# Optimization experiments

Measured on AMD Instinct MI355X. Metric: run time of the kernel, lower is better.

Reference implementation:

```python
import jax, jax.numpy as jnp
import numpy as np

EMBED = 3072
HEADS = 24
HEAD_DIM = EMBED // HEADS
FFN = 4 * EMBED
SEGS = (1024, 2048, 4096)
DILS = (1, 2, 4)
SEQ = 8192
BATCH = 1


def setup_inputs() -> dict:
    key = jax.random.key(0)
    ks = jax.random.split(key, 8)
    E, F = EMBED, FFN
    s = lambda k, shape, sc: (jax.random.normal(k, shape, jnp.float32) * sc)
    return {
        "x": s(ks[0], (BATCH, SEQ, E), 1.0),
        "expert_embed": s(ks[1], (1, 1, E), 0.02),
        "w_qkv": s(ks[2], (3 * E, E), E ** -0.5),
        "b_qkv": jnp.zeros((3 * E,), jnp.float32),
        "w_out": s(ks[3], (E, E), E ** -0.5),
        "b_out": jnp.zeros((E,), jnp.float32),
        "ln1_g": jnp.ones((E,), jnp.float32),
        "ln1_b": jnp.zeros((E,), jnp.float32),
        "w1": s(ks[4], (F, E), E ** -0.5),
        "b1": jnp.zeros((F,), jnp.float32),
        "w2": s(ks[5], (E, F), F ** -0.5),
        "b2": jnp.zeros((E,), jnp.float32),
        "ln2_g": jnp.ones((E,), jnp.float32),
        "ln2_b": jnp.zeros((E,), jnp.float32),
    }


def _layernorm(x, g, b):
    m = jnp.mean(x, axis=-1, keepdims=True)
    v = jnp.mean(jnp.square(x - m), axis=-1, keepdims=True)
    return (x - m) * jax.lax.rsqrt(v + 1e-5) * g + b


def _dilated_attn(q, k, v):
    # q,k,v: [b, n, h, d]; heads are partitioned across dilation groups
    b, n, h, d = q.shape
    G = len(SEGS)
    hg = h // G
    scale = 1.0 / np.sqrt(d)
    outs = []
    for i, (g, r) in enumerate(zip(SEGS, DILS)):
        off = i % r
        hs = slice(i * hg, (i + 1) * hg)

        def sel(t):
            # [b, n, h, d] -> [b, n//g, g//r, hg, d] (dilated segment view)
            return t.reshape(b, n // g, g, h, d)[:, :, off::r, hs, :]

        qi, ki, vi = sel(q), sel(k), sel(v)
        att = jnp.einsum("bsqhd,bskhd->bshqk", qi, ki) * scale
        att = jax.nn.softmax(att, axis=-1)
        oi = jnp.einsum("bshqk,bskhd->bsqhd", att, vi)
        # scatter dilated positions back; unselected positions stay zero
        buf = jnp.zeros((b, n // g, g, hg, d), q.dtype).at[:, :, off::r].set(oi)
        outs.append(buf.reshape(b, n, hg, d))
    return jnp.concatenate(outs, axis=2)  # head groups are contiguous slices


def reference(x, expert_embed, w_qkv, b_qkv, w_out, b_out,
              ln1_g, ln1_b, w1, b1, w2, b2, ln2_g, ln2_b):
    b, n, E = x.shape
    x = x + expert_embed
    qkv = x @ w_qkv.T + b_qkv
    q, k, v = [t.reshape(b, n, HEADS, HEAD_DIM) for t in jnp.split(qkv, 3, axis=-1)]
    a = _dilated_attn(q, k, v).reshape(b, n, E) @ w_out.T + b_out
    x = _layernorm(x + a, ln1_g, ln1_b)
    f = jax.nn.gelu(x @ w1.T + b1, approximate=False) @ w2.T + b2
    return _layernorm(x + f, ln2_g, ln2_b)
```

## Files before the change

kernel.cpp:

```cpp
#include <hip/hip_runtime.h>

typedef unsigned short u16;
typedef __bf16 bf16x8 __attribute__((ext_vector_type(8)));
typedef float f32x4 __attribute__((ext_vector_type(4)));
typedef u16 u16x4 __attribute__((ext_vector_type(4)));
typedef u16 u16x8 __attribute__((ext_vector_type(8)));

__device__ __forceinline__ u16 f2bf(float f) {
  union { float f; unsigned u; } v; v.f = f;
  return (u16)((v.u + 0x7fffu + ((v.u >> 16) & 1u)) >> 16);
}
__device__ __forceinline__ float b2f(u16 h) {
  union { unsigned u; float f; } v; v.u = ((unsigned)h) << 16; return v.f;
}

__device__ __forceinline__ void gld16(const void* g, void* l) {
  __builtin_amdgcn_global_load_lds(
      (const __attribute__((address_space(1))) unsigned int*)g,
      (__attribute__((address_space(3))) unsigned int*)l, 16, 0, 0);
}

#define BAR() asm volatile("s_barrier" ::: "memory")
#define VMC6() asm volatile("s_waitcnt vmcnt(6)" ::: "memory")
#define VMC0() asm volatile("s_waitcnt vmcnt(0)" ::: "memory")

__global__ __launch_bounds__(256) void prep_kernel(const float* __restrict__ x,
                                                   const float* __restrict__ ee,
                                                   u16* __restrict__ xb) {
  size_t i = ((size_t)blockIdx.x * 256 + threadIdx.x) * 4;
  int col = (int)(i % 3072);
  f32x4 v = *(const f32x4*)&x[i];
  f32x4 e = *(const f32x4*)&ee[col];
  v += e;
  u16x4 b = { f2bf(v[0]), f2bf(v[1]), f2bf(v[2]), f2bf(v[3]) };
  *(u16x4*)&xb[i] = b;
}

__global__ __launch_bounds__(256) void cvt_kernel(const float* __restrict__ in,
                                                  u16* __restrict__ out, size_t n) {
  size_t i = ((size_t)blockIdx.x * 256 + threadIdx.x) * 4;
  if (i >= n) return;
  f32x4 v = *(const f32x4*)&in[i];
  u16x4 b = { f2bf(v[0]), f2bf(v[1]), f2bf(v[2]), f2bf(v[3]) };
  *(u16x4*)&out[i] = b;
}

__global__ __launch_bounds__(256) void cvt_strided_kernel(const float* __restrict__ in,
                                                          u16* __restrict__ out, int k0) {
  size_t i = ((size_t)blockIdx.x * 256 + threadIdx.x) * 4;
  int n = (int)(i / 6144), k = (int)(i % 6144);
  f32x4 v = *(const f32x4*)&in[(size_t)n * 12288 + k0 + k];
  u16x4 b = { f2bf(v[0]), f2bf(v[1]), f2bf(v[2]), f2bf(v[3]) };
  *(u16x4*)&out[i] = b;
}

template<int EPI>
__global__ __launch_bounds__(512, 2) void gemmu_kernel(const u16* __restrict__ A,
                                                       const u16* __restrict__ B,
                                                       const float* __restrict__ bias,
                                                       const float* __restrict__ residf,
                                                       const u16* __restrict__ residb,
                                                       const float* __restrict__ ee,
                                                       void* __restrict__ C0,
                                                       void* __restrict__ C1,
                                                       int N, int K) {
  __shared__ __align__(16) u16 lds[73728];
  const int tid = threadIdx.x;
  const int lane = tid & 63;
  const int w = tid >> 6;
  const int lr = lane & 15, lc8 = (lane >> 4) * 8;
  const int wm64 = (w >> 1) * 64;
  const int wn64 = (w & 1) * 64;
  const int rsw = (lr & 7) << 3;

  const int ntile = N >> 7;
  int bid = blockIdx.x;
  int wg = (bid & 7) * (gridDim.x >> 3) + (bid >> 3);
  const int bm = wg / ntile, bn = wg % ntile;
  const size_t m0 = (size_t)bm << 8, n0 = (size_t)bn << 7;

  const int jsw = (tid & 7) ^ ((tid >> 3) & 7);
  const u16* gA = A + (m0 + (tid >> 3)) * (size_t)K + jsw * 8;
  const u16* gB = B + (n0 + (tid >> 3)) * (size_t)K + jsw * 8;
  u16* lA = &lds[tid * 8];
  u16* lB = &lds[16384 + tid * 8];

  f32x4 acc[4][4] = {};
  bf16x8 af[2][4], bfr[2][4];

  const int NT = K >> 6;

  auto stageA2 = [&](int buf, int kk) {
    gld16(gA + kk, lA + buf * 24576);
    gld16(gA + (size_t)64 * K + kk, lA + buf * 24576 + 64 * 64);
    gld16(gA + (size_t)128 * K + kk, lA + buf * 24576 + 128 * 64);
    gld16(gA + (size_t)192 * K + kk, lA + buf * 24576 + 192 * 64);
  };
  auto stageB2 = [&](int buf, int kk) {
    gld16(gB + kk, lB + buf * 24576);
    gld16(gB + (size_t)64 * K + kk, lB + buf * 24576 + 64 * 64);
  };
  auto LA = [&](int buf) {
#pragma unroll
    for (int ks = 0; ks < 2; ++ks)
#pragma unroll
      for (int f = 0; f < 4; ++f) {
        int r = wm64 + f * 16 + lr;
        af[ks][f] = *(const bf16x8*)&lds[buf * 24576 + r * 64 + ((ks * 32 + lc8) ^ rsw)];
      }
  };
  auto LBall = [&](int buf) {
#pragma unroll
    for (int ks = 0; ks < 2; ++ks)
#pragma unroll
      for (int f = 0; f < 4; ++f) {
        int r = wn64 + f * 16 + lr;
        bfr[ks][f] = *(const bf16x8*)&lds[buf * 24576 + 16384 + r * 64 + ((ks * 32 + lc8) ^ rsw)];
      }
  };
  auto MMA = [&]() {
    __builtin_amdgcn_s_setprio(1);
#pragma unroll
    for (int ks = 0; ks < 2; ++ks)
#pragma unroll
      for (int f = 0; f < 4; ++f)
#pragma unroll
        for (int f2 = 0; f2 < 4; ++f2)
          acc[f][f2] = __builtin_amdgcn_mfma_f32_16x16x32_bf16(
              af[ks][f], bfr[ks][f2], acc[f][f2], 0, 0, 0);
    __builtin_amdgcn_s_setprio(0);
  };
  auto TILE = [&](int bc, int bs, int tt) {
    const int kk2 = (tt + 2) << 6;
    const bool p = (tt + 2) < NT;
    LA(bc); LBall(bc);
    if (p) { stageA2(bs, kk2); stageB2(bs, kk2); }
    MMA();
    if (p) { VMC6(); } else { VMC0(); }
    BAR();
  };

  stageA2(0, 0); stageB2(0, 0);
  stageA2(1, 64); stageB2(1, 64);
  VMC6();
  BAR();

  for (int t = 0; t < NT; t += 3) {
    TILE(0, 2, t);
    TILE(1, 0, t + 1);
    TILE(2, 1, t + 2);
  }

  const int ldc = (EPI == 7) ? 3072 : N;
#pragma unroll
  for (int nf = 0; nf < 4; ++nf) {
    const int colL = wn64 + nf * 16 + lr;
    const size_t col = n0 + colL;
    float bv = 0.f;
    if constexpr (EPI != 9) bv = bias[col];
    const int ci = colL >> 3;
#pragma unroll
    for (int f = 0; f < 4; ++f) {
#pragma unroll
      for (int rg = 0; rg < 4; ++rg) {
        const int rowL = wm64 + f * 16 + (lc8 >> 1) + rg;
        const size_t idx = (m0 + rowL) * (size_t)N + col;
        float v = acc[f][nf][rg] + bv;
        if constexpr (EPI == 2)
          v = 0.5f * v * (1.0f + erff(v * 0.7071067811865476f));
        if constexpr (EPI == 3) v += residf[idx] + ee[col];
        if constexpr (EPI == 8) v += b2f(residb[idx]);
        if constexpr (EPI == 9) v += b2f(((const u16*)C0)[idx]);
        const int fz = (rowL >> 2) & 7;
        lds[rowL * 128 + (((ci ^ fz) << 3) | (colL & 7))] = f2bf(v);
      }
    }
  }
  __syncthreads();
  const int row = tid >> 1, half = tid & 1;
  const int fro = (row >> 2) & 7;
  u16* dst;
  size_t cb;
  if constexpr (EPI == 7) {
    const int sec = (n0 >= 3072);
    dst = sec ? (u16*)C1 : (u16*)C0;
    cb = n0 - (sec ? 3072 : 0);
  } else {
    dst = (u16*)C0; cb = n0;
  }
  u16* gout = dst + (m0 + row) * (size_t)ldc + cb + half * 64;
#pragma unroll
  for (int i = 0; i < 8; ++i) {
    const int ci = half * 8 + i;
    *(uint4*)&gout[i * 8] = *(const uint4*)&lds[row * 128 + ((ci ^ fro) << 3)];
  }
}

__device__ __forceinline__ void decode_blk(int bid, int& grp, int& g, int& r, int& off,
                                           int& q16, int& hl, int& s) {
  if (bid < 1024)      { grp = 0; g = 1024; r = 1; off = 0; }
  else if (bid < 1536) { grp = 1; g = 2048; r = 2; off = 1; bid -= 1024; }
  else                 { grp = 2; g = 4096; r = 4; off = 2; bid -= 1536; }
  q16 = bid & 15; hl = (bid >> 4) & 7; s = bid >> 7;
}

__global__ __launch_bounds__(256) void vtrans_kernel(const u16* __restrict__ Vb,
                                                     u16* __restrict__ vtd) {
  int grp, g, r, off, jb, hl, s;
  decode_blk(blockIdx.x, grp, g, r, off, jb, hl, s);
  const int h = grp * 8 + hl;
  const size_t vbase = (size_t)((grp == 0) ? 0u : (grp == 1) ? 8388608u : 12582912u)
                       + (size_t)(s * 8 + hl) * 131072;
  __shared__ u16 t[64 * 128];
  const int tid = threadIdx.x;
#pragma unroll
  for (int i = 0; i < 4; ++i) {
    int c = tid + i * 256;
    int jj = c >> 4, c16 = c & 15;
    size_t pos = (size_t)s * g + off + (size_t)(jb * 64 + jj) * r;
    uint4 d = *(const uint4*)&Vb[pos * 3072 + h * 128 + c16 * 8];
    *(uint4*)((char*)t + jj * 256 + ((c16 * 16) ^ ((jj >> 3) << 4))) = d;
  }
  __syncthreads();
#pragma unroll
  for (int i = 0; i < 4; ++i) {
    int c = tid + i * 256;
    int dd = c >> 3, jc = c & 7;
    u16x8 vals;
#pragma unroll
    for (int q = 0; q < 8; ++q) {
      int row = jc * 8 + q;
      vals[q] = *(const u16*)((const char*)t + row * 256 + ((dd * 2) ^ (jc << 4)));
    }
    *(u16x8*)&vtd[vbase + (size_t)dd * 1024 + jb * 64 + jc * 8] = vals;
  }
}

__global__ __launch_bounds__(256) void attn_kernel(const u16* __restrict__ Qb,
                                                   const u16* __restrict__ Kb,
                                                   const u16* __restrict__ vtd,
                                                   u16* __restrict__ abuf) {
  int grp, g, r, off, qt, hl, s;
  decode_blk(blockIdx.x, grp, g, r, off, qt, hl, s);
  const int h = grp * 8 + hl;
  const size_t vbase = (size_t)((grp == 0) ? 0u : (grp == 1) ? 8388608u : 12582912u)
                       + (size_t)(s * 8 + hl) * 131072;
  const size_t segoff = (size_t)s * g + off;

  const int tid = threadIdx.x;
  const int lane = tid & 63, w = tid >> 6;
  const int lr = lane & 15, lc = lane >> 4;

  __shared__ u16 Kl[64 * 128];
  __shared__ u16 Vl[128 * 64];
  __shared__ u16 Pl[4][1024];

  const size_t qpos = segoff + (size_t)(qt * 64 + w * 16 + lr) * r;
  const u16* qrow = &Qb[qpos * 3072 + h * 128];
  bf16x8 qf[4];
#pragma unroll
  for (int kc = 0; kc < 4; ++kc) qf[kc] = *(const bf16x8*)&qrow[kc * 32 + lc * 8];

  float m_run[4], l_run[4];
  f32x4 ao[8] = {};
#pragma unroll
  for (int i = 0; i < 4; ++i) { m_run[i] = -1e30f; l_run[i] = 0.f; }

  const float scale = 0.08838834764831845f;

  for (int kt = 0; kt < 16; ++kt) {
    __syncthreads();
#pragma unroll
    for (int i = 0; i < 4; ++i) {
      int c = tid + i * 256;
      int jj = c >> 4, c16 = c & 15;
      size_t kpos = segoff + (size_t)(kt * 64 + jj) * r;
      uint4 kd = *(const uint4*)&Kb[kpos * 3072 + h * 128 + c16 * 8];
      *(uint4*)((char*)Kl + jj * 256 + ((c16 * 16) ^ ((jj & 7) << 4))) = kd;
      int dd = c >> 3, jc = c & 7;
      uint4 vd = *(const uint4*)&vtd[vbase + (size_t)dd * 1024 + kt * 64 + jc * 8];
      *(uint4*)((char*)Vl + dd * 128 + ((jc * 16) ^ ((dd & 7) << 4))) = vd;
    }
    __syncthreads();

    f32x4 sc4[4] = {};
#pragma unroll
    for (int kb = 0; kb < 4; ++kb) {
      const int key = kb * 16 + lr;
      const int swz = (key & 7) << 4;
#pragma unroll
      for (int kc = 0; kc < 4; ++kc) {
        bf16x8 kf = *(const bf16x8*)((const char*)Kl + key * 256 + ((kc * 64 + lc * 16) ^ swz));
        sc4[kb] = __builtin_amdgcn_mfma_f32_16x16x32_bf16(qf[kc], kf, sc4[kb], 0, 0, 0);
      }
    }

    float pv[4][4];
#pragma unroll
    for (int rg = 0; rg < 4; ++rg) {
      float t = fmaxf(fmaxf(sc4[0][rg], sc4[1][rg]), fmaxf(sc4[2][rg], sc4[3][rg]));
#pragma unroll
      for (int sh = 1; sh < 16; sh <<= 1) t = fmaxf(t, __shfl_xor(t, sh, 64));
      t *= scale;
      const float mn = fmaxf(m_run[rg], t);
      const float corr = __expf(m_run[rg] - mn);
      m_run[rg] = mn;
      float sum = 0.f;
#pragma unroll
      for (int kb = 0; kb < 4; ++kb) {
        float p = __expf(sc4[kb][rg] * scale - mn);
        pv[kb][rg] = p; sum += p;
      }
#pragma unroll
      for (int sh = 1; sh < 16; sh <<= 1) sum += __shfl_xor(sum, sh, 64);
      l_run[rg] = l_run[rg] * corr + sum;
#pragma unroll
      for (int nb = 0; nb < 8; ++nb) ao[nb][rg] *= corr;
    }

#pragma unroll
    for (int rg = 0; rg < 4; ++rg) {
      const int q = lc * 4 + rg;
      const int swq = (q & 7) << 4;
#pragma unroll
      for (int kb = 0; kb < 4; ++kb) {
        const int key = kb * 16 + lr;
        *(u16*)((char*)&Pl[w][0] + q * 128 + ((key * 2) ^ swq)) = f2bf(pv[kb][rg]);
      }
    }
    __syncthreads();

#pragma unroll
    for (int kc2 = 0; kc2 < 2; ++kc2) {
      bf16x8 pf = *(const bf16x8*)((const char*)&Pl[w][0] + lr * 128 + ((kc2 * 64 + lc * 16) ^ ((lr & 7) << 4)));
#pragma unroll
      for (int nb = 0; nb < 8; ++nb) {
        const int dd = nb * 16 + lr;
        bf16x8 vf = *(const bf16x8*)((const char*)Vl + dd * 128 + ((kc2 * 64 + lc * 16) ^ ((dd & 7) << 4)));
        ao[nb] = __builtin_amdgcn_mfma_f32_16x16x32_bf16(pf, vf, ao[nb], 0, 0, 0);
      }
    }
  }

#pragma unroll
  for (int rg = 0; rg < 4; ++rg) {
    const float inv = 1.f / l_run[rg];
    const size_t opos = segoff + (size_t)(qt * 64 + w * 16 + lc * 4 + rg) * r;
    u16* orow = &abuf[opos * 3072 + h * 128];
#pragma unroll
    for (int nb = 0; nb < 8; ++nb) orow[nb * 16 + lr] = f2bf(ao[nb][rg] * inv);
  }
}

template<int IN_BF, int OUT_BF>
__global__ __launch_bounds__(256) void ln_kernel(const void* __restrict__ yv,
                                                 const float* __restrict__ gm,
                                                 const float* __restrict__ bt,
                                                 void* __restrict__ outv) {
  const size_t row = blockIdx.x;
  const int tid = threadIdx.x;
  float v[12];
  float s = 0.f, ss = 0.f;
#pragma unroll
  for (int i = 0; i < 3; ++i) {
    if constexpr (IN_BF) {
      u16x4 raw = *(const u16x4*)((const u16*)yv + row * 3072 + tid * 4 + i * 1024);
#pragma unroll
      for (int j = 0; j < 4; ++j) { float f = b2f(raw[j]); v[i * 4 + j] = f; s += f; ss += f * f; }
    } else {
      f32x4 raw = *(const f32x4*)((const float*)yv + row * 3072 + tid * 4 + i * 1024);
#pragma unroll
      for (int j = 0; j < 4; ++j) { float f = raw[j]; v[i * 4 + j] = f; s += f; ss += f * f; }
    }
  }
#pragma unroll
  for (int sh = 1; sh < 64; sh <<= 1) { s += __shfl_xor(s, sh, 64); ss += __shfl_xor(ss, sh, 64); }
  __shared__ float red[8];
  if ((tid & 63) == 0) { red[tid >> 6] = s; red[4 + (tid >> 6)] = ss; }
  __syncthreads();
  s = red[0] + red[1] + red[2] + red[3];
  ss = red[4] + red[5] + red[6] + red[7];
  const float mean = s * (1.f / 3072.f);
  const float var = ss * (1.f / 3072.f) - mean * mean;
  const float rs = rsqrtf(var + 1e-5f);
#pragma unroll
  for (int i = 0; i < 3; ++i) {
    int c = tid * 4 + i * 1024;
    f32x4 g4 = *(const f32x4*)&gm[c];
    f32x4 b4 = *(const f32x4*)&bt[c];
    if constexpr (OUT_BF) {
      u16x4 ob;
#pragma unroll
      for (int j = 0; j < 4; ++j) ob[j] = f2bf((v[i * 4 + j] - mean) * rs * g4[j] + b4[j]);
      *(u16x4*)((u16*)outv + row * 3072 + c) = ob;
    } else {
      f32x4 o;
#pragma unroll
      for (int j = 0; j < 4; ++j) o[j] = (v[i * 4 + j] - mean) * rs * g4[j] + b4[j];
      *(f32x4*)((float*)outv + row * 3072 + c) = o;
    }
  }
}

extern "C" void kernel_launch(void* const* d_in, const int* in_sizes, int n_in,
                              void* d_out, int out_size, void* d_ws, size_t ws_size,
                              hipStream_t stream) {
  (void)in_sizes; (void)n_in; (void)out_size;
  const float* x    = (const float*)d_in[0];
  const float* ee   = (const float*)d_in[1];
  const float* wqkv = (const float*)d_in[2];
  const float* bqkv = (const float*)d_in[3];
  const float* wout = (const float*)d_in[4];
  const float* bout = (const float*)d_in[5];
  const float* ln1g = (const float*)d_in[6];
  const float* ln1b = (const float*)d_in[7];
  const float* w1   = (const float*)d_in[8];
  const float* b1   = (const float*)d_in[9];
  const float* w2   = (const float*)d_in[10];
  const float* b2   = (const float*)d_in[11];
  const float* ln2g = (const float*)d_in[12];
  const float* ln2b = (const float*)d_in[13];
  float* out = (float*)d_out;

  static const size_t OFF_B1  = 50331648;
  static const size_t OFF_B2  = 100663296;
  static const size_t WS_NEED = 150994944;
  if (ws_size < WS_NEED) return;

  char* ws = (char*)d_ws;
  u16*   xb    = (u16*)(ws);
  u16*   vtd   = (u16*)(ws);
  u16*   wbo   = (u16*)(ws);
  u16*   x1b   = (u16*)(ws);
  u16*   Qb    = (u16*)(ws + OFF_B1);
  u16*   y1b   = (u16*)(ws + OFF_B1);
  u16*   y2b   = (u16*)(ws + OFF_B1);
  u16*   wslot = (u16*)(ws + OFF_B2);
  u16*   abuf  = (u16*)(ws + OFF_B2);
  u16*   Kb    = (u16*)d_out;
  u16*   Vb    = (u16*)((char*)d_out + 50331648);
  u16*   hcd   = (u16*)d_out;

  prep_kernel<<<24576, 256, 0, stream>>>(x, ee, xb);

  cvt_kernel<<<18432, 256, 0, stream>>>(wqkv, wslot, 18874368);
  gemmu_kernel<7><<<1536, 512, 0, stream>>>(xb, wslot, bqkv, nullptr, nullptr, nullptr,
                                            Qb, Kb, 6144, 3072);
  cvt_kernel<<<9216, 256, 0, stream>>>(wqkv + 18874368, wslot, 9437184);
  gemmu_kernel<0><<<768, 512, 0, stream>>>(xb, wslot, bqkv + 6144, nullptr, nullptr, nullptr,
                                           Vb, nullptr, 3072, 3072);

  vtrans_kernel<<<1792, 256, 0, stream>>>(Vb, vtd);
  hipMemsetAsync(abuf, 0, 50331648, stream);
  attn_kernel<<<1792, 256, 0, stream>>>(Qb, Kb, vtd, abuf);

  cvt_kernel<<<9216, 256, 0, stream>>>(wout, wbo, 9437184);
  gemmu_kernel<3><<<768, 512, 0, stream>>>(abuf, wbo, bout, x, nullptr, ee,
                                           y1b, nullptr, 3072, 3072);
  ln_kernel<1, 1><<<8192, 256, 0, stream>>>(y1b, ln1g, ln1b, x1b);

  for (int c = 0; c < 2; ++c) {
    cvt_kernel<<<18432, 256, 0, stream>>>(w1 + (size_t)c * 18874368, wslot, 18874368);
    gemmu_kernel<2><<<1536, 512, 0, stream>>>(x1b, wslot, b1 + c * 6144, nullptr, nullptr, nullptr,
                                              hcd, nullptr, 6144, 3072);
    cvt_strided_kernel<<<18432, 256, 0, stream>>>(w2, wslot, c * 6144);
    if (c == 0)
      gemmu_kernel<8><<<768, 512, 0, stream>>>(hcd, wslot, b2, nullptr, x1b, nullptr,
                                               y2b, nullptr, 3072, 6144);
    else
      gemmu_kernel<9><<<768, 512, 0, stream>>>(hcd, wslot, b2, nullptr, nullptr, nullptr,
                                               y2b, nullptr, 3072, 6144);
  }

  ln_kernel<1, 0><<<8192, 256, 0, stream>>>(y2b, ln2g, ln2b, out);
}
```

Before: 2.276 ms.

## Switch GEMM to BK=32 stages with higher occupancy and direct epilogue stores

Replaces the GEMM's 64-wide K stages with 32-wide stages, halving LDS use so that four workgroups can fit per CU instead of two. It uses a new paired-row LDS swizzle and changes the XCD-aware tile mapping so each XCD owns a band of N tiles. The LDS-staged coalesced epilogue is replaced by direct scalar bf16 global stores. This trades per-iteration barrier overhead and uncoalesced 2-byte writes for more occupancy and better L2 reuse of B.

```diff
diff --git a/kernel.cpp b/kernel.cpp
--- a/kernel.cpp
+++ b/kernel.cpp
@@ -21,7 +21,7 @@
 }
 
 #define BAR() asm volatile("s_barrier" ::: "memory")
-#define VMC6() asm volatile("s_waitcnt vmcnt(6)" ::: "memory")
+#define VMC3() asm volatile("s_waitcnt vmcnt(3)" ::: "memory")
 #define VMC0() asm volatile("s_waitcnt vmcnt(0)" ::: "memory")
 
 __global__ __launch_bounds__(256) void prep_kernel(const float* __restrict__ x,
@@ -55,94 +55,92 @@
 }
 
 template<int EPI>
-__global__ __launch_bounds__(512, 2) void gemmu_kernel(const u16* __restrict__ A,
-                                                       const u16* __restrict__ B,
-                                                       const float* __restrict__ bias,
-                                                       const float* __restrict__ residf,
-                                                       const u16* __restrict__ residb,
-                                                       const float* __restrict__ ee,
-                                                       void* __restrict__ C0,
-                                                       void* __restrict__ C1,
-                                                       int N, int K) {
-  __shared__ __align__(16) u16 lds[73728];
+__global__ __launch_bounds__(512, 4) void gemm32_kernel(const u16* __restrict__ A,
+                                                        const u16* __restrict__ B,
+                                                        const float* __restrict__ bias,
+                                                        const float* __restrict__ residf,
+                                                        const u16* __restrict__ residb,
+                                                        const float* __restrict__ ee,
+                                                        void* __restrict__ C0,
+                                                        void* __restrict__ C1,
+                                                        int N, int K) {
+  __shared__ __align__(16) u16 lds[36864];
   const int tid = threadIdx.x;
   const int lane = tid & 63;
   const int w = tid >> 6;
-  const int lr = lane & 15, lc8 = (lane >> 4) * 8;
+  const int lr = lane & 15;
+  const int lc = lane >> 4;
   const int wm64 = (w >> 1) * 64;
   const int wn64 = (w & 1) * 64;
-  const int rsw = (lr & 7) << 3;
 
   const int ntile = N >> 7;
-  int bid = blockIdx.x;
-  int wg = (bid & 7) * (gridDim.x >> 3) + (bid >> 3);
-  const int bm = wg / ntile, bn = wg % ntile;
+  const int nper = ntile >> 3;
+  const int bid = blockIdx.x;
+  const int xcd = bid & 7;
+  const int local = bid >> 3;
+  const int bn = xcd * nper + local % nper;
+  const int bm = local / nper;
   const size_t m0 = (size_t)bm << 8, n0 = (size_t)bn << 7;
 
-  const int jsw = (tid & 7) ^ ((tid >> 3) & 7);
-  const u16* gA = A + (m0 + (tid >> 3)) * (size_t)K + jsw * 8;
-  const u16* gB = B + (n0 + (tid >> 3)) * (size_t)K + jsw * 8;
+  const int sl = tid >> 3;
+  const int srow = sl * 2 + ((tid >> 2) & 1);
+  const int scol = ((tid & 3) ^ (sl & 3)) * 8;
+  const u16* gA = A + (m0 + srow) * (size_t)K + scol;
+  const u16* gB = B + (n0 + srow) * (size_t)K + scol;
   u16* lA = &lds[tid * 8];
-  u16* lB = &lds[16384 + tid * 8];
+  u16* lB = &lds[8192 + tid * 8];
 
   f32x4 acc[4][4] = {};
-  bf16x8 af[2][4], bfr[2][4];
-
-  const int NT = K >> 6;
-
-  auto stageA2 = [&](int buf, int kk) {
-    gld16(gA + kk, lA + buf * 24576);
-    gld16(gA + (size_t)64 * K + kk, lA + buf * 24576 + 64 * 64);
-    gld16(gA + (size_t)128 * K + kk, lA + buf * 24576 + 128 * 64);
-    gld16(gA + (size_t)192 * K + kk, lA + buf * 24576 + 192 * 64);
-  };
-  auto stageB2 = [&](int buf, int kk) {
-    gld16(gB + kk, lB + buf * 24576);
-    gld16(gB + (size_t)64 * K + kk, lB + buf * 24576 + 64 * 64);
+  bf16x8 af[4], bfr[4];
+
+  const int NT = K >> 5;
+
+  auto stageA = [&](int buf, int kk) {
+    gld16(gA + kk, lA + buf * 12288);
+    gld16(gA + (size_t)128 * K + kk, lA + buf * 12288 + 4096);
+  };
+  auto stageB = [&](int buf, int kk) {
+    gld16(gB + kk, lB + buf * 12288);
   };
   auto LA = [&](int buf) {
 #pragma unroll
-    for (int ks = 0; ks < 2; ++ks)
-#pragma unroll
-      for (int f = 0; f < 4; ++f) {
-        int r = wm64 + f * 16 + lr;
-        af[ks][f] = *(const bf16x8*)&lds[buf * 24576 + r * 64 + ((ks * 32 + lc8) ^ rsw)];
-      }
-  };
-  auto LBall = [&](int buf) {
-#pragma unroll
-    for (int ks = 0; ks < 2; ++ks)
-#pragma unroll
-      for (int f = 0; f < 4; ++f) {
-        int r = wn64 + f * 16 + lr;
-        bfr[ks][f] = *(const bf16x8*)&lds[buf * 24576 + 16384 + r * 64 + ((ks * 32 + lc8) ^ rsw)];
-      }
+    for (int f = 0; f < 4; ++f) {
+      int r = wm64 + f * 16 + lr;
+      int p = r >> 1;
+      af[f] = *(const bf16x8*)&lds[buf * 12288 + p * 64 + (r & 1) * 32 + ((lc ^ (p & 3)) << 3)];
+    }
+  };
+  auto LB = [&](int buf) {
+#pragma unroll
+    for (int f = 0; f < 4; ++f) {
+      int r = wn64 + f * 16 + lr;
+      int p = r >> 1;
+      bfr[f] = *(const bf16x8*)&lds[buf * 12288 + 8192 + p * 64 + (r & 1) * 32 + ((lc ^ (p & 3)) << 3)];
+    }
   };
   auto MMA = [&]() {
     __builtin_amdgcn_s_setprio(1);
 #pragma unroll
-    for (int ks = 0; ks < 2; ++ks)
-#pragma unroll
-      for (int f = 0; f < 4; ++f)
-#pragma unroll
-        for (int f2 = 0; f2 < 4; ++f2)
-          acc[f][f2] = __builtin_amdgcn_mfma_f32_16x16x32_bf16(
-              af[ks][f], bfr[ks][f2], acc[f][f2], 0, 0, 0);
+    for (int f = 0; f < 4; ++f)
+#pragma unroll
+      for (int f2 = 0; f2 < 4; ++f2)
+        acc[f][f2] = __builtin_amdgcn_mfma_f32_16x16x32_bf16(
+            af[f], bfr[f2], acc[f][f2], 0, 0, 0);
     __builtin_amdgcn_s_setprio(0);
   };
   auto TILE = [&](int bc, int bs, int tt) {
-    const int kk2 = (tt + 2) << 6;
+    const int kk2 = (tt + 2) << 5;
     const bool p = (tt + 2) < NT;
-    LA(bc); LBall(bc);
-    if (p) { stageA2(bs, kk2); stageB2(bs, kk2); }
+    LA(bc); LB(bc);
+    if (p) { stageA(bs, kk2); stageB(bs, kk2); }
     MMA();
-    if (p) { VMC6(); } else { VMC0(); }
+    if (p) { VMC3(); } else { VMC0(); }
     BAR();
   };
 
-  stageA2(0, 0); stageB2(0, 0);
-  stageA2(1, 64); stageB2(1, 64);
-  VMC6();
+  stageA(0, 0); stageB(0, 0);
+  stageA(1, 32); stageB(1, 32);
+  VMC3();
   BAR();
 
   for (int t = 0; t < NT; t += 3) {
@@ -151,48 +149,37 @@
     TILE(2, 1, t + 2);
   }
 
-  const int ldc = (EPI == 7) ? 3072 : N;
 #pragma unroll
   for (int nf = 0; nf < 4; ++nf) {
-    const int colL = wn64 + nf * 16 + lr;
-    const size_t col = n0 + colL;
+    const size_t col = n0 + wn64 + nf * 16 + lr;
     float bv = 0.f;
     if constexpr (EPI != 9) bv = bias[col];
-    const int ci = colL >> 3;
+    u16* dstb;
+    size_t colw = col;
+    int ldc;
+    if constexpr (EPI == 7) {
+      const int sec = (int)(col / 3072);
+      dstb = sec ? (u16*)C1 : (u16*)C0;
+      colw = col - (size_t)sec * 3072;
+      ldc = 3072;
+    } else {
+      dstb = (u16*)C0; ldc = N;
+    }
 #pragma unroll
     for (int f = 0; f < 4; ++f) {
 #pragma unroll
       for (int rg = 0; rg < 4; ++rg) {
-        const int rowL = wm64 + f * 16 + (lc8 >> 1) + rg;
-        const size_t idx = (m0 + rowL) * (size_t)N + col;
+        const size_t row = m0 + wm64 + f * 16 + lc * 4 + rg;
+        const size_t idx = row * ldc + colw;
         float v = acc[f][nf][rg] + bv;
         if constexpr (EPI == 2)
           v = 0.5f * v * (1.0f + erff(v * 0.7071067811865476f));
-        if constexpr (EPI == 3) v += residf[idx] + ee[col];
-        if constexpr (EPI == 8) v += b2f(residb[idx]);
+        if constexpr (EPI == 3) v += residf[row * (size_t)N + col] + ee[col];
+        if constexpr (EPI == 8) v += b2f(residb[row * (size_t)N + col]);
         if constexpr (EPI == 9) v += b2f(((const u16*)C0)[idx]);
-        const int fz = (rowL >> 2) & 7;
-        lds[rowL * 128 + (((ci ^ fz) << 3) | (colL & 7))] = f2bf(v);
+        dstb[idx] = f2bf(v);
       }
     }
-  }
-  __syncthreads();
-  const int row = tid >> 1, half = tid & 1;
-  const int fro = (row >> 2) & 7;
-  u16* dst;
-  size_t cb;
-  if constexpr (EPI == 7) {
-    const int sec = (n0 >= 3072);
-    dst = sec ? (u16*)C1 : (u16*)C0;
-    cb = n0 - (sec ? 3072 : 0);
-  } else {
-    dst = (u16*)C0; cb = n0;
-  }
-  u16* gout = dst + (m0 + row) * (size_t)ldc + cb + half * 64;
-#pragma unroll
-  for (int i = 0; i < 8; ++i) {
-    const int ci = half * 8 + i;
-    *(uint4*)&gout[i * 8] = *(const uint4*)&lds[row * 128 + ((ci ^ fro) << 3)];
   }
 }
 
@@ -444,32 +431,32 @@
   prep_kernel<<<24576, 256, 0, stream>>>(x, ee, xb);
 
   cvt_kernel<<<18432, 256, 0, stream>>>(wqkv, wslot, 18874368);
-  gemmu_kernel<7><<<1536, 512, 0, stream>>>(xb, wslot, bqkv, nullptr, nullptr, nullptr,
-                                            Qb, Kb, 6144, 3072);
+  gemm32_kernel<7><<<1536, 512, 0, stream>>>(xb, wslot, bqkv, nullptr, nullptr, nullptr,
+                                             Qb, Kb, 6144, 3072);
   cvt_kernel<<<9216, 256, 0, stream>>>(wqkv + 18874368, wslot, 9437184);
-  gemmu_kernel<0><<<768, 512, 0, stream>>>(xb, wslot, bqkv + 6144, nullptr, nullptr, nullptr,
-                                           Vb, nullptr, 3072, 3072);
+  gemm32_kernel<0><<<768, 512, 0, stream>>>(xb, wslot, bqkv + 6144, nullptr, nullptr, nullptr,
+                                            Vb, nullptr, 3072, 3072);
 
   vtrans_kernel<<<1792, 256, 0, stream>>>(Vb, vtd);
   hipMemsetAsync(abuf, 0, 50331648, stream);
   attn_kernel<<<1792, 256, 0, stream>>>(Qb, Kb, vtd, abuf);
 
   cvt_kernel<<<9216, 256, 0, stream>>>(wout, wbo, 9437184);
-  gemmu_kernel<3><<<768, 512, 0, stream>>>(abuf, wbo, bout, x, nullptr, ee,
-                                           y1b, nullptr, 3072, 3072);
+  gemm32_kernel<3><<<768, 512, 0, stream>>>(abuf, wbo, bout, x, nullptr, ee,
+                                            y1b, nullptr, 3072, 3072);
   ln_kernel<1, 1><<<8192, 256, 0, stream>>>(y1b, ln1g, ln1b, x1b);
 
   for (int c = 0; c < 2; ++c) {
     cvt_kernel<<<18432, 256, 0, stream>>>(w1 + (size_t)c * 18874368, wslot, 18874368);
-    gemmu_kernel<2><<<1536, 512, 0, stream>>>(x1b, wslot, b1 + c * 6144, nullptr, nullptr, nullptr,
-                                              hcd, nullptr, 6144, 3072);
+    gemm32_kernel<2><<<1536, 512, 0, stream>>>(x1b, wslot, b1 + c * 6144, nullptr, nullptr, nullptr,
+                                               hcd, nullptr, 6144, 3072);
     cvt_strided_kernel<<<18432, 256, 0, stream>>>(w2, wslot, c * 6144);
     if (c == 0)
-      gemmu_kernel<8><<<768, 512, 0, stream>>>(hcd, wslot, b2, nullptr, x1b, nullptr,
-                                               y2b, nullptr, 3072, 6144);
+      gemm32_kernel<8><<<768, 512, 0, stream>>>(hcd, wslot, b2, nullptr, x1b, nullptr,
+                                                y2b, nullptr, 3072, 6144);
     else
-      gemmu_kernel<9><<<768, 512, 0, stream>>>(hcd, wslot, b2, nullptr, nullptr, nullptr,
-                                               y2b, nullptr, 3072, 6144);
+      gemm32_kernel<9><<<768, 512, 0, stream>>>(hcd, wslot, b2, nullptr, nullptr, nullptr,
+                                                y2b, nullptr, 3072, 6144);
   }
 
   ln_kernel<1, 0><<<8192, 256, 0, stream>>>(y2b, ln2g, ln2b, out);
```

New measurement: 4.033 ms. 77.2% more time.

## Fuse weight conversions into tails of preceding kernels and chunk FFN into quarters

Applied to the files above, without the earlier changes.

Standalone fp32→bf16 weight conversion launches are removed, and the conversion of the next weight chunk is appended as a grid-stride tail to the preceding GEMM or attention kernel, using double-buffered slots in the output buffer. The QKV GEMM is split into separate Q and K launches, the FFN is processed in four 3072-wide chunks instead of two, and GEMM block-to-tile mapping is changed so each XCD owns a contiguous set of N tiles. The intent is to cut launch count and let conversion traffic overlap with compute tails. The trade-off is extra tail work in the GEMM kernels, more GEMM launches with smaller K for the second FFN GEMM, and reliance on nper = ntile/8 being an integer.

```diff
diff --git a/kernel.cpp b/kernel.cpp
--- a/kernel.cpp
+++ b/kernel.cpp
@@ -23,6 +23,25 @@
 #define BAR() asm volatile("s_barrier" ::: "memory")
 #define VMC6() asm volatile("s_waitcnt vmcnt(6)" ::: "memory")
 #define VMC0() asm volatile("s_waitcnt vmcnt(0)" ::: "memory")
+
+__device__ __forceinline__ void cvt_tail_c(const float* __restrict__ src,
+                                           u16* __restrict__ dst, int gtid, int gsz) {
+  for (int i = gtid; i < 2359296; i += gsz) {
+    f32x4 v = *(const f32x4*)(src + (size_t)i * 4);
+    u16x4 b = { f2bf(v[0]), f2bf(v[1]), f2bf(v[2]), f2bf(v[3]) };
+    *(u16x4*)(dst + (size_t)i * 4) = b;
+  }
+}
+__device__ __forceinline__ void cvt_tail_s(const float* __restrict__ src,
+                                           u16* __restrict__ dst, int k04,
+                                           int gtid, int gsz) {
+  for (int i = gtid; i < 2359296; i += gsz) {
+    int n = i / 768, cc = i - n * 768;
+    f32x4 v = *(const f32x4*)(src + ((size_t)n * 3072 + k04 + cc) * 4);
+    u16x4 b = { f2bf(v[0]), f2bf(v[1]), f2bf(v[2]), f2bf(v[3]) };
+    *(u16x4*)(dst + (size_t)i * 4) = b;
+  }
+}
 
 __global__ __launch_bounds__(256) void prep_kernel(const float* __restrict__ x,
                                                    const float* __restrict__ ee,
@@ -45,15 +64,6 @@
   *(u16x4*)&out[i] = b;
 }
 
-__global__ __launch_bounds__(256) void cvt_strided_kernel(const float* __restrict__ in,
-                                                          u16* __restrict__ out, int k0) {
-  size_t i = ((size_t)blockIdx.x * 256 + threadIdx.x) * 4;
-  int n = (int)(i / 6144), k = (int)(i % 6144);
-  f32x4 v = *(const f32x4*)&in[(size_t)n * 12288 + k0 + k];
-  u16x4 b = { f2bf(v[0]), f2bf(v[1]), f2bf(v[2]), f2bf(v[3]) };
-  *(u16x4*)&out[i] = b;
-}
-
 template<int EPI>
 __global__ __launch_bounds__(512, 2) void gemmu_kernel(const u16* __restrict__ A,
                                                        const u16* __restrict__ B,
@@ -62,8 +72,12 @@
                                                        const u16* __restrict__ residb,
                                                        const float* __restrict__ ee,
                                                        void* __restrict__ C0,
-                                                       void* __restrict__ C1,
-                                                       int N, int K) {
+                                                       int N, int K,
+                                                       const float* __restrict__ cs1,
+                                                       u16* __restrict__ cd1,
+                                                       const float* __restrict__ cs2,
+                                                       u16* __restrict__ cd2,
+                                                       int ck04) {
   __shared__ __align__(16) u16 lds[73728];
   const int tid = threadIdx.x;
   const int lane = tid & 63;
@@ -74,9 +88,12 @@
   const int rsw = (lr & 7) << 3;
 
   const int ntile = N >> 7;
-  int bid = blockIdx.x;
-  int wg = (bid & 7) * (gridDim.x >> 3) + (bid >> 3);
-  const int bm = wg / ntile, bn = wg % ntile;
+  const int nper = ntile >> 3;
+  const int bid = blockIdx.x;
+  const int xcd = bid & 7;
+  const int local = bid >> 3;
+  const int bn = xcd * nper + local % nper;
+  const int bm = local / nper;
   const size_t m0 = (size_t)bm << 8, n0 = (size_t)bn << 7;
 
   const int jsw = (tid & 7) ^ ((tid >> 3) & 7);
@@ -151,7 +168,6 @@
     TILE(2, 1, t + 2);
   }
 
-  const int ldc = (EPI == 7) ? 3072 : N;
 #pragma unroll
   for (int nf = 0; nf < 4; ++nf) {
     const int colL = wn64 + nf * 16 + lr;
@@ -179,21 +195,17 @@
   __syncthreads();
   const int row = tid >> 1, half = tid & 1;
   const int fro = (row >> 2) & 7;
-  u16* dst;
-  size_t cb;
-  if constexpr (EPI == 7) {
-    const int sec = (n0 >= 3072);
-    dst = sec ? (u16*)C1 : (u16*)C0;
-    cb = n0 - (sec ? 3072 : 0);
-  } else {
-    dst = (u16*)C0; cb = n0;
-  }
-  u16* gout = dst + (m0 + row) * (size_t)ldc + cb + half * 64;
+  u16* gout = (u16*)C0 + (m0 + row) * (size_t)N + n0 + half * 64;
 #pragma unroll
   for (int i = 0; i < 8; ++i) {
     const int ci = half * 8 + i;
     *(uint4*)&gout[i * 8] = *(const uint4*)&lds[row * 128 + ((ci ^ fro) << 3)];
   }
+
+  const int gtid = bid * 512 + tid;
+  const int gsz = (int)gridDim.x * 512;
+  if (cd1) cvt_tail_c(cs1, cd1, gtid, gsz);
+  if (cd2) cvt_tail_s(cs2, cd2, ck04, gtid, gsz);
 }
 
 __device__ __forceinline__ void decode_blk(int bid, int& grp, int& g, int& r, int& off,
@@ -239,7 +251,9 @@
 __global__ __launch_bounds__(256) void attn_kernel(const u16* __restrict__ Qb,
                                                    const u16* __restrict__ Kb,
                                                    const u16* __restrict__ vtd,
-                                                   u16* __restrict__ abuf) {
+                                                   u16* __restrict__ abuf,
+                                                   const float* __restrict__ csrc,
+                                                   u16* __restrict__ cdst) {
   int grp, g, r, off, qt, hl, s;
   decode_blk(blockIdx.x, grp, g, r, off, qt, hl, s);
   const int h = grp * 8 + hl;
@@ -350,6 +364,8 @@
 #pragma unroll
     for (int nb = 0; nb < 8; ++nb) orow[nb * 16 + lr] = f2bf(ao[nb][rg] * inv);
   }
+
+  if (cdst) cvt_tail_c(csrc, cdst, blockIdx.x * 256 + tid, 1792 * 256);
 }
 
 template<int IN_BF, int OUT_BF>
@@ -430,46 +446,63 @@
   char* ws = (char*)d_ws;
   u16*   xb    = (u16*)(ws);
   u16*   vtd   = (u16*)(ws);
-  u16*   wbo   = (u16*)(ws);
   u16*   x1b   = (u16*)(ws);
   u16*   Qb    = (u16*)(ws + OFF_B1);
   u16*   y1b   = (u16*)(ws + OFF_B1);
   u16*   y2b   = (u16*)(ws + OFF_B1);
   u16*   wslot = (u16*)(ws + OFF_B2);
   u16*   abuf  = (u16*)(ws + OFF_B2);
-  u16*   Kb    = (u16*)d_out;
-  u16*   Vb    = (u16*)((char*)d_out + 50331648);
-  u16*   hcd   = (u16*)d_out;
+  u16*   hc    = (u16*)(ws + OFF_B2);
+
+  u16* Kb    = (u16*)d_out;
+  u16* Vb    = (u16*)d_out + 25165824;
+  u16* woutb = (u16*)d_out + 25165824;
+  u16* sW1[2] = { (u16*)d_out + 0,        (u16*)d_out + 18874368 };
+  u16* sW2[2] = { (u16*)d_out + 9437184,  (u16*)d_out + 28311552 };
 
   prep_kernel<<<24576, 256, 0, stream>>>(x, ee, xb);
 
   cvt_kernel<<<18432, 256, 0, stream>>>(wqkv, wslot, 18874368);
-  gemmu_kernel<7><<<1536, 512, 0, stream>>>(xb, wslot, bqkv, nullptr, nullptr, nullptr,
-                                            Qb, Kb, 6144, 3072);
+  gemmu_kernel<0><<<768, 512, 0, stream>>>(xb, wslot, bqkv, nullptr, nullptr, nullptr,
+                                           Qb, 3072, 3072,
+                                           nullptr, nullptr, nullptr, nullptr, 0);
+  gemmu_kernel<0><<<768, 512, 0, stream>>>(xb, wslot + 9437184, bqkv + 3072, nullptr, nullptr, nullptr,
+                                           Kb, 3072, 3072,
+                                           nullptr, nullptr, nullptr, nullptr, 0);
   cvt_kernel<<<9216, 256, 0, stream>>>(wqkv + 18874368, wslot, 9437184);
   gemmu_kernel<0><<<768, 512, 0, stream>>>(xb, wslot, bqkv + 6144, nullptr, nullptr, nullptr,
-                                           Vb, nullptr, 3072, 3072);
+                                           Vb, 3072, 3072,
+                                           nullptr, nullptr, nullptr, nullptr, 0);
 
   vtrans_kernel<<<1792, 256, 0, stream>>>(Vb, vtd);
   hipMemsetAsync(abuf, 0, 50331648, stream);
-  attn_kernel<<<1792, 256, 0, stream>>>(Qb, Kb, vtd, abuf);
-
-  cvt_kernel<<<9216, 256, 0, stream>>>(wout, wbo, 9437184);
-  gemmu_kernel<3><<<768, 512, 0, stream>>>(abuf, wbo, bout, x, nullptr, ee,
-                                           y1b, nullptr, 3072, 3072);
+  attn_kernel<<<1792, 256, 0, stream>>>(Qb, Kb, vtd, abuf, wout, woutb);
+
+  gemmu_kernel<3><<<768, 512, 0, stream>>>(abuf, woutb, bout, x, nullptr, ee,
+                                           y1b, 3072, 3072,
+                                           w1, sW1[0], w2, sW2[0], 0);
   ln_kernel<1, 1><<<8192, 256, 0, stream>>>(y1b, ln1g, ln1b, x1b);
 
-  for (int c = 0; c < 2; ++c) {
-    cvt_kernel<<<18432, 256, 0, stream>>>(w1 + (size_t)c * 18874368, wslot, 18874368);
-    gemmu_kernel<2><<<1536, 512, 0, stream>>>(x1b, wslot, b1 + c * 6144, nullptr, nullptr, nullptr,
-                                              hcd, nullptr, 6144, 3072);
-    cvt_strided_kernel<<<18432, 256, 0, stream>>>(w2, wslot, c * 6144);
+  for (int c = 0; c < 4; ++c) {
+    const int p = c & 1;
+    const bool more = (c < 3);
+    gemmu_kernel<2><<<768, 512, 0, stream>>>(x1b, sW1[p], b1 + c * 3072, nullptr, nullptr, nullptr,
+                                             hc, 3072, 3072,
+                                             more ? (w1 + (size_t)(c + 1) * 9437184) : nullptr,
+                                             more ? sW1[1 - p] : nullptr,
+                                             nullptr, nullptr, 0);
     if (c == 0)
-      gemmu_kernel<8><<<768, 512, 0, stream>>>(hcd, wslot, b2, nullptr, x1b, nullptr,
-                                               y2b, nullptr, 3072, 6144);
+      gemmu_kernel<8><<<768, 512, 0, stream>>>(hc, sW2[0], b2, nullptr, x1b, nullptr,
+                                               y2b, 3072, 3072,
+                                               nullptr, nullptr,
+                                               w2, sW2[1], 768);
     else
-      gemmu_kernel<9><<<768, 512, 0, stream>>>(hcd, wslot, b2, nullptr, nullptr, nullptr,
-                                               y2b, nullptr, 3072, 6144);
+      gemmu_kernel<9><<<768, 512, 0, stream>>>(hc, sW2[p], b2, nullptr, nullptr, nullptr,
+                                               y2b, 3072, 3072,
+                                               nullptr, nullptr,
+                                               more ? w2 : nullptr,
+                                               more ? sW2[1 - p] : nullptr,
+                                               (c + 1) * 768);
   }
 
   ln_kernel<1, 0><<<8192, 256, 0, stream>>>(y2b, ln2g, ln2b, out);
```

Result: slower. 2.363 ms (+3.8%).
